# Performance work log

Hardware: AMD Instinct MI355X
Metric: run time of the kernel (lower is better)

The kernel has to match this reference:

```python
import jax, jax.numpy as jnp
import numpy as np
import math

DIM = 512
HID = 2048
BS, SLEN = 4, 4096


def _bayes_linear(x, mu, log_sigma, eps):
    # torchbnn BayesLinear: W = mu + exp(log_sigma) * eps; y = x @ W^T
    W = mu + jnp.exp(log_sigma) * eps
    return jnp.einsum('...i,oi->...o', x, W)


def setup_inputs() -> dict:
    key = jax.random.key(0)
    ks = jax.random.split(key, 20)
    d = {}
    d['x'] = jax.random.normal(ks[0], (BS, SLEN, DIM), dtype=jnp.float32)
    # causal additive mask, broadcast over batch
    causal = jnp.triu(jnp.full((SLEN, SLEN), -1e9, dtype=jnp.float32), k=1)
    d['mask'] = causal[None, :, :]
    shapes = {'wk': (DIM, DIM), 'wv': (DIM, DIM), 'wo': (DIM, DIM), 'w1': (HID, DIM), 'w2': (DIM, HID)}
    i = 1
    for name, shp in shapes.items():
        fan_in = shp[1]
        d[name + '_mu'] = jax.random.normal(ks[i], shp, dtype=jnp.float32) / np.sqrt(fan_in); i += 1
        d[name + '_ls'] = (-3.0 + 0.1 * jax.random.normal(ks[i], shp, dtype=jnp.float32)); i += 1
        d[name + '_eps'] = jax.random.normal(ks[i], shp, dtype=jnp.float32); i += 1
    return d


def reference(x, mask, wk_mu, wk_ls, wk_eps, wv_mu, wv_ls, wv_eps, wo_mu, wo_ls, wo_eps,
              w1_mu, w1_ls, w1_eps, w2_mu, w2_ls, w2_eps):
    dim = x.shape[-1]
    # attention: W_q is identity
    xq = x
    xk = _bayes_linear(x, wk_mu, wk_ls, wk_eps)
    xv = _bayes_linear(x, wv_mu, wv_ls, wv_eps)
    scores = jnp.einsum('bqd,bkd->bqk', xq, xk) / math.sqrt(dim) + mask
    attn = jax.nn.softmax(scores, axis=-1)
    h = jnp.einsum('bqk,bkd->bqd', attn, xv)
    h_attn = _bayes_linear(h, wo_mu, wo_ls, wo_eps)
    h_res = x + h_attn
    # FFN with ReLU
    ff = _bayes_linear(h_res, w1_mu, w1_ls, w1_eps)
    ff = jax.nn.relu(ff)
    ff = _bayes_linear(ff, w2_mu, w2_ls, w2_eps)
    return h_res + ff
```

## Files before the change

### kernel.cpp

```cpp
#include <hip/hip_runtime.h>
#include <hip/hip_bf16.h>

typedef __hip_bfloat16 bf16;
typedef __attribute__((ext_vector_type(8))) short short8;
typedef __attribute__((ext_vector_type(4))) float f32x4;

#define MFMA16(a,b,c) __builtin_amdgcn_mfma_f32_16x16x32_bf16(a,b,c,0,0,0)

__device__ __forceinline__ void gl_lds16(const void* g, void* l) {
  __builtin_amdgcn_global_load_lds(
      (const __attribute__((address_space(1))) void*)g,
      (__attribute__((address_space(3))) void*)l, 16, 0, 0);
}

__global__ __launch_bounds__(256) void prep_kernel(
    const float* __restrict__ x,
    const float* __restrict__ m0, const float* __restrict__ l0, const float* __restrict__ e0,
    const float* __restrict__ m1, const float* __restrict__ l1, const float* __restrict__ e1,
    const float* __restrict__ m2, const float* __restrict__ l2, const float* __restrict__ e2,
    const float* __restrict__ m3, const float* __restrict__ l3, const float* __restrict__ e3,
    const float* __restrict__ m4, const float* __restrict__ l4, const float* __restrict__ e4,
    bf16* __restrict__ xb, bf16* __restrict__ wts)
{
  long e = ((long)blockIdx.x * 256 + threadIdx.x) * 4;
  if (e < 8388608L) {
    float4 v = *(const float4*)(x + e);
    union { bf16 b[4]; short4 s; } u;
    u.b[0] = __float2bfloat16(v.x); u.b[1] = __float2bfloat16(v.y);
    u.b[2] = __float2bfloat16(v.z); u.b[3] = __float2bfloat16(v.w);
    *(short4*)(xb + e) = u.s;
  } else {
    long we = e - 8388608L;
    const float *mu, *ls, *ep; long off = we;
    if (we < 262144L)        { mu = m0; ls = l0; ep = e0; }
    else if (we < 524288L)   { mu = m1; ls = l1; ep = e1; off = we - 262144L; }
    else if (we < 786432L)   { mu = m2; ls = l2; ep = e2; off = we - 524288L; }
    else if (we < 1835008L)  { mu = m3; ls = l3; ep = e3; off = we - 786432L; }
    else                     { mu = m4; ls = l4; ep = e4; off = we - 1835008L; }
    float4 a = *(const float4*)(mu + off);
    float4 b = *(const float4*)(ls + off);
    float4 c = *(const float4*)(ep + off);
    union { bf16 w[4]; short4 s; } u;
    u.w[0] = __float2bfloat16(a.x + __expf(b.x) * c.x);
    u.w[1] = __float2bfloat16(a.y + __expf(b.y) * c.y);
    u.w[2] = __float2bfloat16(a.z + __expf(b.z) * c.z);
    u.w[3] = __float2bfloat16(a.w + __expf(b.w) * c.w);
    *(short4*)(wts + we) = u.s;
  }
}

template<int MODE>
__global__ __launch_bounds__(256, 2) void gemm_nt(
    const bf16* __restrict__ A, const bf16* __restrict__ B,
    const float* __restrict__ resid, float* __restrict__ outf,
    bf16* __restrict__ outb, int M, int N, int K)
{
  __shared__ bf16 As[128 * 32];
  __shared__ bf16 Bs[128 * 32];
  const int t = threadIdx.x, w = t >> 6, lane = t & 63;
  const int quad = lane >> 4, c16 = lane & 15;
  const int bm = blockIdx.x << 7, bn = blockIdx.y << 7;
  const int wr = (w >> 1) << 6, wc = (w & 1) << 6;

  f32x4 acc[4][4] = {};

  const int srow = t >> 2;
  const int scol = (t & 3) * 8;
  const bf16* Ab = A + (long)bm * K;
  const bf16* Bb = B + (long)bn * K;

  for (int k0 = 0; k0 < K; k0 += 32) {
    gl_lds16(Ab + (long)srow * K + k0 + scol,        (char*)As + (w << 10));
    gl_lds16(Ab + (long)(64 + srow) * K + k0 + scol, (char*)As + 4096 + (w << 10));
    gl_lds16(Bb + (long)srow * K + k0 + scol,        (char*)Bs + (w << 10));
    gl_lds16(Bb + (long)(64 + srow) * K + k0 + scol, (char*)Bs + 4096 + (w << 10));
    __syncthreads();
    short8 a[4], b[4];
    #pragma unroll
    for (int i = 0; i < 4; i++)
      a[i] = *(const short8*)(As + (wr + i * 16 + c16) * 32 + quad * 8);
    #pragma unroll
    for (int j = 0; j < 4; j++)
      b[j] = *(const short8*)(Bs + (wc + j * 16 + c16) * 32 + quad * 8);
    #pragma unroll
    for (int i = 0; i < 4; i++)
      #pragma unroll
      for (int j = 0; j < 4; j++)
        acc[i][j] = MFMA16(a[i], b[j], acc[i][j]);
    __syncthreads();
  }

  #pragma unroll
  for (int i = 0; i < 4; i++) {
    const int row = bm + wr + i * 16 + quad * 4;
    #pragma unroll
    for (int j = 0; j < 4; j++) {
      const int col = bn + wc + j * 16 + c16;
      #pragma unroll
      for (int r = 0; r < 4; r++) {
        float v = acc[i][j][r];
        if (MODE == 4) {
          int n = (row + r) & 31;
          long idx = (long)(row + r) * 512 + ((((col >> 3) ^ (n & 7)) << 3) | (col & 7));
          outb[idx] = __float2bfloat16(v);
        } else if (MODE == 5) {
          int g = row + r;
          int kvl = g & 31;
          long idx = (((long)(g >> 5)) << 14) + (long)col * 32 +
                     (((kvl >> 3) ^ ((col >> 1) & 3)) << 3) + (kvl & 7);
          outb[idx] = __float2bfloat16(v);
        } else {
          long idx = (long)(row + r) * N + col;
          if (MODE == 0) {
            outb[idx] = __float2bfloat16(v);
          } else if (MODE == 1) {
            float vv = v + resid[idx];
            outf[idx] = vv;
            outb[idx] = __float2bfloat16(vv);
          } else if (MODE == 2) {
            outb[idx] = __float2bfloat16(v > 0.f ? v : 0.f);
          } else {
            outf[idx] = v + resid[idx];
          }
        }
      }
    }
  }
}

__global__ __launch_bounds__(256, 2) void attn4_kernel(
    const bf16* __restrict__ xq, const bf16* __restrict__ xkS,
    const bf16* __restrict__ xvS, bf16* __restrict__ Opart,
    float* __restrict__ lsum)
{
  __shared__ bf16 Ks[32 * 512];
  __shared__ bf16 Vs[512 * 32];
  __shared__ bf16 Pb[4 * 512];

  const int t = threadIdx.x, w = t >> 6, lane = t & 63;
  const int quad = lane >> 4, c16 = lane & 15;
  const int n = blockIdx.x;
  const int B = n & 3, par = (n >> 2) & 3, i = n >> 4;
  const long boff = (long)B * (4096L * 512);
  const float scale = 0.04419417382415922f;
  const float FM = 30.0f;

  union { short8 s; short u[8]; } ones;
  #pragma unroll
  for (int k = 0; k < 8; k++) ones.u[k] = (short)0x3F80;

  for (int seg = 0; seg < 2; seg++) {
    const int qt = seg ? (63 - i) : i;
    const int T = 2 * (qt + 1);
    const int qb = qt << 6;

    short8 qf[16];
    {
      const bf16* qrow = xq + boff + (long)(qb + w * 16 + c16) * 512 + quad * 8;
      #pragma unroll
      for (int f = 0; f < 16; f++) qf[f] = *(const short8*)(qrow + f * 32);
    }

    f32x4 o[32];
    #pragma unroll
    for (int jj = 0; jj < 32; jj++) o[jj] = (f32x4){0.f, 0.f, 0.f, 0.f};
    f32x4 lacc = (f32x4){0.f, 0.f, 0.f, 0.f};

    for (int tile = par; tile < T; tile += 4) {
      const int kv0 = tile << 5;
      {
        const long tb = ((long)(B * 128 + tile)) << 14;
        const bf16* ks = xkS + tb + (w << 9) + (lane << 3);
        const bf16* vs = xvS + tb + (w << 9) + (lane << 3);
        char* kd = (char*)Ks + (w << 10);
        char* vd = (char*)Vs + (w << 10);
        #pragma unroll
        for (int r2 = 0; r2 < 8; r2++) {
          gl_lds16(ks + (r2 << 11), kd + (r2 << 12));
          gl_lds16(vs + (r2 << 11), vd + (r2 << 12));
        }
      }
      __syncthreads();

      f32x4 s0 = (f32x4){0.f, 0.f, 0.f, 0.f};
      f32x4 s1 = s0;
      const int n0 = c16, n1 = 16 + c16;
      const int sw0 = (c16 & 7) << 3;
      #pragma unroll
      for (int f = 0; f < 16; f++) {
        int cb = (f * 4 + quad) << 3;
        short8 b0 = *(const short8*)(Ks + n0 * 512 + (cb ^ sw0));
        short8 b1 = *(const short8*)(Ks + n1 * 512 + (cb ^ sw0));
        s0 = MFMA16(qf[f], b0, s0);
        s1 = MFMA16(qf[f], b1, s1);
      }

      bf16* Pw = Pb + (w << 9);
      {
        const int qr0 = qb + w * 16 + quad * 4;
        const bool need_mask = (kv0 + 32 > qb);
        #pragma unroll
        for (int r = 0; r < 4; r++) {
          float p0 = __expf(fmaf(s0[r], scale, -FM));
          float p1 = __expf(fmaf(s1[r], scale, -FM));
          if (need_mask) {
            if (kv0 + n0 > qr0 + r) p0 = 0.f;
            if (kv0 + n1 > qr0 + r) p1 = 0.f;
          }
          int pr = quad * 4 + r;
          int swp = (pr >> 1) & 3;
          Pw[pr * 32 + (((n0 >> 3) ^ swp) << 3) + (n0 & 7)] = __float2bfloat16(p0);
          Pw[pr * 32 + (((n1 >> 3) ^ swp) << 3) + (n1 & 7)] = __float2bfloat16(p1);
        }
      }
      short8 pa = *(const short8*)(Pw + c16 * 32 + ((quad ^ ((c16 >> 1) & 3)) << 3));
      lacc = MFMA16(pa, ones.s, lacc);
      #pragma unroll
      for (int jj = 0; jj < 32; jj++) {
        int d = jj * 16 + c16;
        short8 vb = *(const short8*)(Vs + d * 32 + ((quad ^ ((d >> 1) & 3)) << 3));
        o[jj] = MFMA16(pa, vb, o[jj]);
      }
      __syncthreads();
    }

    const int pidx = (B * 64 + qt) * 4 + par;
    {
      bf16* ob = Opart + ((long)pidx << 15) + (long)(w * 16 + quad * 4) * 512 + c16;
      #pragma unroll
      for (int r = 0; r < 4; r++) {
        #pragma unroll
        for (int jj = 0; jj < 32; jj++)
          ob[(long)r * 512 + jj * 16] = __float2bfloat16(o[jj][r]);
      }
      if (c16 == 0) {
        #pragma unroll
        for (int r = 0; r < 4; r++)
          lsum[pidx * 64 + w * 16 + quad * 4 + r] = lacc[r];
      }
    }
  }
}

__global__ __launch_bounds__(256) void combine_kernel(
    const bf16* __restrict__ Opart, const float* __restrict__ lsum,
    bf16* __restrict__ hb)
{
  const int t = threadIdx.x;
  const int r = blockIdx.x * 4 + (t >> 6);
  const int B = r >> 12, rl = r & 4095, qt = rl >> 6, rr = rl & 63;
  const int p0 = (B * 64 + qt) * 4;
  float lt = lsum[p0 * 64 + rr] + lsum[(p0 + 1) * 64 + rr] +
             lsum[(p0 + 2) * 64 + rr] + lsum[(p0 + 3) * 64 + rr];
  float inv = 1.0f / lt;
  const int d0 = (t & 63) * 8;
  union { short8 s; bf16 b[8]; } u0, u1, u2, u3, uo;
  u0.s = *(const short8*)(Opart + (((long)(p0 + 0) << 6) + rr) * 512 + d0);
  u1.s = *(const short8*)(Opart + (((long)(p0 + 1) << 6) + rr) * 512 + d0);
  u2.s = *(const short8*)(Opart + (((long)(p0 + 2) << 6) + rr) * 512 + d0);
  u3.s = *(const short8*)(Opart + (((long)(p0 + 3) << 6) + rr) * 512 + d0);
  #pragma unroll
  for (int k = 0; k < 8; k++) {
    float s = __bfloat162float(u0.b[k]) + __bfloat162float(u1.b[k]) +
              __bfloat162float(u2.b[k]) + __bfloat162float(u3.b[k]);
    uo.b[k] = __float2bfloat16(s * inv);
  }
  *(short8*)(hb + (long)r * 512 + d0) = uo.s;
}

extern "C" void kernel_launch(void* const* d_in, const int* in_sizes, int n_in,
                              void* d_out, int out_size, void* d_ws, size_t ws_size,
                              hipStream_t stream) {
  (void)in_sizes; (void)n_in; (void)out_size; (void)ws_size;
  const float* x = (const float*)d_in[0];
  const float* wk_mu = (const float*)d_in[2],  *wk_ls = (const float*)d_in[3],  *wk_eps = (const float*)d_in[4];
  const float* wv_mu = (const float*)d_in[5],  *wv_ls = (const float*)d_in[6],  *wv_eps = (const float*)d_in[7];
  const float* wo_mu = (const float*)d_in[8],  *wo_ls = (const float*)d_in[9],  *wo_eps = (const float*)d_in[10];
  const float* w1_mu = (const float*)d_in[11], *w1_ls = (const float*)d_in[12], *w1_eps = (const float*)d_in[13];
  const float* w2_mu = (const float*)d_in[14], *w2_ls = (const float*)d_in[15], *w2_eps = (const float*)d_in[16];

  const long MB = 1048576L;
  char* ws = (char*)d_ws;
  bf16*   xb    = (bf16*)(ws + 0);
  bf16*   xkS   = (bf16*)(ws + 16 * MB);
  bf16*   xvS   = (bf16*)(ws + 32 * MB);
  bf16*   Opart = (bf16*)(ws + 48 * MB);
  float*  lsb   = (float*)(ws + 112 * MB);
  bf16*   wts   = (bf16*)(ws + 113 * MB);
  bf16*   hb    = (bf16*)(ws + 32 * MB);
  float*  hrf   = (float*)(ws + 64 * MB);
  bf16*   hrb   = (bf16*)(ws + 96 * MB);
  bf16*   ffb   = (bf16*)(ws + 0);

  bf16* wkb = wts;
  bf16* wvb = wts + 262144;
  bf16* wob = wts + 524288;
  bf16* w1b = wts + 786432;
  bf16* w2b = wts + 1835008;

  prep_kernel<<<11008, 256, 0, stream>>>(x,
      wk_mu, wk_ls, wk_eps, wv_mu, wv_ls, wv_eps, wo_mu, wo_ls, wo_eps,
      w1_mu, w1_ls, w1_eps, w2_mu, w2_ls, w2_eps, xb, wts);

  gemm_nt<4><<<dim3(128, 4),  256, 0, stream>>>(xb,  wkb, nullptr, nullptr, xkS, 16384, 512, 512);
  gemm_nt<5><<<dim3(128, 4),  256, 0, stream>>>(xb,  wvb, nullptr, nullptr, xvS, 16384, 512, 512);

  attn4_kernel<<<512, 256, 0, stream>>>(xb, xkS, xvS, Opart, lsb);
  combine_kernel<<<4096, 256, 0, stream>>>(Opart, lsb, hb);

  gemm_nt<1><<<dim3(128, 4),  256, 0, stream>>>(hb,  wob, x,   hrf, hrb, 16384, 512, 512);
  gemm_nt<2><<<dim3(128, 16), 256, 0, stream>>>(hrb, w1b, nullptr, nullptr, ffb, 16384, 2048, 512);
  gemm_nt<3><<<dim3(128, 4),  256, 0, stream>>>(ffb, w2b, hrf, (float*)d_out, nullptr, 16384, 512, 2048);
}
```

Baseline: 464.6 us.

## Prefetch next K/V tiles during compute and split PV output across waves by column

The attention kernel now loads the next tile's K into LDS while the current PV product runs, and the next V right after it finishes, so global-to-LDS loads overlap with MFMA work. The PV product is repartitioned: each wave reads the P tiles of all four waves from LDS and owns a 128-column slice of the output for all 64 rows. Each V fragment is then read from LDS once and reused across four row blocks, instead of every wave reading all of V. This adds extra barriers and P reads per tile, and it changes the Opart write pattern.

```diff
diff --git a/kernel.cpp b/kernel.cpp
--- a/kernel.cpp
+++ b/kernel.cpp
@@ -128,7 +128,7 @@
   }
 }
 
-__global__ __launch_bounds__(256, 2) void attn4_kernel(
+__global__ __launch_bounds__(256, 2) void attn5_kernel(
     const bf16* __restrict__ xq, const bf16* __restrict__ xkS,
     const bf16* __restrict__ xvS, bf16* __restrict__ Opart,
     float* __restrict__ lsum)
@@ -149,6 +149,21 @@
   #pragma unroll
   for (int k = 0; k < 8; k++) ones.u[k] = (short)0x3F80;
 
+  auto stageK = [&](int tile) {
+    const long tb = ((long)(B * 128 + tile)) << 14;
+    const bf16* ks = xkS + tb + (w << 9) + (lane << 3);
+    char* kd = (char*)Ks + (w << 10);
+    #pragma unroll
+    for (int r2 = 0; r2 < 8; r2++) gl_lds16(ks + (r2 << 11), kd + (r2 << 12));
+  };
+  auto stageV = [&](int tile) {
+    const long tb = ((long)(B * 128 + tile)) << 14;
+    const bf16* vs = xvS + tb + (w << 9) + (lane << 3);
+    char* vd = (char*)Vs + (w << 10);
+    #pragma unroll
+    for (int r2 = 0; r2 < 8; r2++) gl_lds16(vs + (r2 << 11), vd + (r2 << 12));
+  };
+
   for (int seg = 0; seg < 2; seg++) {
     const int qt = seg ? (63 - i) : i;
     const int T = 2 * (qt + 1);
@@ -161,25 +176,17 @@
       for (int f = 0; f < 16; f++) qf[f] = *(const short8*)(qrow + f * 32);
     }
 
-    f32x4 o[32];
-    #pragma unroll
-    for (int jj = 0; jj < 32; jj++) o[jj] = (f32x4){0.f, 0.f, 0.f, 0.f};
+    f32x4 o[4][8];
+    #pragma unroll
+    for (int rb = 0; rb < 4; rb++)
+      #pragma unroll
+      for (int db = 0; db < 8; db++) o[rb][db] = (f32x4){0.f, 0.f, 0.f, 0.f};
     f32x4 lacc = (f32x4){0.f, 0.f, 0.f, 0.f};
+
+    if (par < T) { stageK(par); stageV(par); }
 
     for (int tile = par; tile < T; tile += 4) {
       const int kv0 = tile << 5;
-      {
-        const long tb = ((long)(B * 128 + tile)) << 14;
-        const bf16* ks = xkS + tb + (w << 9) + (lane << 3);
-        const bf16* vs = xvS + tb + (w << 9) + (lane << 3);
-        char* kd = (char*)Ks + (w << 10);
-        char* vd = (char*)Vs + (w << 10);
-        #pragma unroll
-        for (int r2 = 0; r2 < 8; r2++) {
-          gl_lds16(ks + (r2 << 11), kd + (r2 << 12));
-          gl_lds16(vs + (r2 << 11), vd + (r2 << 12));
-        }
-      }
       __syncthreads();
 
       f32x4 s0 = (f32x4){0.f, 0.f, 0.f, 0.f};
@@ -195,8 +202,8 @@
         s1 = MFMA16(qf[f], b1, s1);
       }
 
-      bf16* Pw = Pb + (w << 9);
       {
+        bf16* Pw = Pb + (w << 9);
         const int qr0 = qb + w * 16 + quad * 4;
         const bool need_mask = (kv0 + 32 > qb);
         #pragma unroll
@@ -213,25 +220,45 @@
           Pw[pr * 32 + (((n1 >> 3) ^ swp) << 3) + (n1 & 7)] = __float2bfloat16(p1);
         }
       }
-      short8 pa = *(const short8*)(Pw + c16 * 32 + ((quad ^ ((c16 >> 1) & 3)) << 3));
-      lacc = MFMA16(pa, ones.s, lacc);
-      #pragma unroll
-      for (int jj = 0; jj < 32; jj++) {
-        int d = jj * 16 + c16;
-        short8 vb = *(const short8*)(Vs + d * 32 + ((quad ^ ((d >> 1) & 3)) << 3));
-        o[jj] = MFMA16(pa, vb, o[jj]);
-      }
       __syncthreads();
+      const bool nxt = (tile + 4) < T;
+      if (nxt) stageK(tile + 4);
+
+      {
+        const int prd = ((quad ^ ((c16 >> 1) & 3)) << 3);
+        short8 pf[4];
+        #pragma unroll
+        for (int rb = 0; rb < 4; rb++)
+          pf[rb] = *(const short8*)(Pb + (rb << 9) + c16 * 32 + prd);
+        short8 pown = *(const short8*)(Pb + (w << 9) + c16 * 32 + prd);
+        lacc = MFMA16(pown, ones.s, lacc);
+        #pragma unroll
+        for (int db = 0; db < 8; db++) {
+          int d = (w << 7) + (db << 4) + c16;
+          short8 vb = *(const short8*)(Vs + d * 32 + ((quad ^ ((d >> 1) & 3)) << 3));
+          #pragma unroll
+          for (int rb = 0; rb < 4; rb++)
+            o[rb][db] = MFMA16(pf[rb], vb, o[rb][db]);
+        }
+      }
+      __syncthreads();
+      if (nxt) stageV(tile + 4);
     }
 
     const int pidx = (B * 64 + qt) * 4 + par;
     {
-      bf16* ob = Opart + ((long)pidx << 15) + (long)(w * 16 + quad * 4) * 512 + c16;
-      #pragma unroll
-      for (int r = 0; r < 4; r++) {
-        #pragma unroll
-        for (int jj = 0; jj < 32; jj++)
-          ob[(long)r * 512 + jj * 16] = __float2bfloat16(o[jj][r]);
+      bf16* ob = Opart + ((long)pidx << 15);
+      #pragma unroll
+      for (int rb = 0; rb < 4; rb++) {
+        #pragma unroll
+        for (int r = 0; r < 4; r++) {
+          const int row = rb * 16 + quad * 4 + r;
+          #pragma unroll
+          for (int db = 0; db < 8; db++) {
+            const int col = (w << 7) + (db << 4) + c16;
+            ob[(long)row * 512 + col] = __float2bfloat16(o[rb][db][r]);
+          }
+        }
       }
       if (c16 == 0) {
         #pragma unroll
@@ -239,6 +266,7 @@
           lsum[pidx * 64 + w * 16 + quad * 4 + r] = lacc[r];
       }
     }
+    __syncthreads();
   }
 }
 
@@ -305,7 +333,7 @@
   gemm_nt<4><<<dim3(128, 4),  256, 0, stream>>>(xb,  wkb, nullptr, nullptr, xkS, 16384, 512, 512);
   gemm_nt<5><<<dim3(128, 4),  256, 0, stream>>>(xb,  wvb, nullptr, nullptr, xvS, 16384, 512, 512);
 
-  attn4_kernel<<<512, 256, 0, stream>>>(xb, xkS, xvS, Opart, lsb);
+  attn5_kernel<<<512, 256, 0, stream>>>(xb, xkS, xvS, Opart, lsb);
   combine_kernel<<<4096, 256, 0, stream>>>(Opart, lsb, hb);
 
   gemm_nt<1><<<dim3(128, 4),  256, 0, stream>>>(hb,  wob, x,   hrf, hrb, 16384, 512, 512);
```

Measured after the change: 538.2 us. 1.16x slower.

## Double GEMM K-tile to 64 with XOR-swizzled LDS layout

Applied to the files above, without the earlier changes.

The NT GEMM now stages a 128x64 K-slice of A and B per iteration instead of 128x32. This halves the number of barrier pairs and loop iterations, and each sync is followed by 32 MFMAs per wave. The 16-byte chunks are XOR-swizzled by row when loaded into LDS so that the fragment reads avoid bank conflicts. LDS use doubles to 32 KB per block, which may limit occupancy with two blocks per CU. The kernel also assumes K is a multiple of 64.

```diff
diff --git a/kernel.cpp b/kernel.cpp
--- a/kernel.cpp
+++ b/kernel.cpp
@@ -55,8 +55,8 @@
     const float* __restrict__ resid, float* __restrict__ outf,
     bf16* __restrict__ outb, int M, int N, int K)
 {
-  __shared__ bf16 As[128 * 32];
-  __shared__ bf16 Bs[128 * 32];
+  __shared__ bf16 As[128 * 64];
+  __shared__ bf16 Bs[128 * 64];
   const int t = threadIdx.x, w = t >> 6, lane = t & 63;
   const int quad = lane >> 4, c16 = lane & 15;
   const int bm = blockIdx.x << 7, bn = blockIdx.y << 7;
@@ -64,29 +64,37 @@
 
   f32x4 acc[4][4] = {};
 
-  const int srow = t >> 2;
-  const int scol = (t & 3) * 8;
+  const int lh = lane >> 3, l8 = lane & 7;
+  const int gcol = (l8 ^ lh) << 3;
   const bf16* Ab = A + (long)bm * K;
   const bf16* Bb = B + (long)bn * K;
 
-  for (int k0 = 0; k0 < K; k0 += 32) {
-    gl_lds16(Ab + (long)srow * K + k0 + scol,        (char*)As + (w << 10));
-    gl_lds16(Ab + (long)(64 + srow) * K + k0 + scol, (char*)As + 4096 + (w << 10));
-    gl_lds16(Bb + (long)srow * K + k0 + scol,        (char*)Bs + (w << 10));
-    gl_lds16(Bb + (long)(64 + srow) * K + k0 + scol, (char*)Bs + 4096 + (w << 10));
+  for (int k0 = 0; k0 < K; k0 += 64) {
+    #pragma unroll
+    for (int r2 = 0; r2 < 4; r2++) {
+      const int R0 = r2 * 32 + w * 8;
+      gl_lds16(Ab + (long)(R0 + lh) * K + k0 + gcol, (char*)As + R0 * 128);
+      gl_lds16(Bb + (long)(R0 + lh) * K + k0 + gcol, (char*)Bs + R0 * 128);
+    }
     __syncthreads();
-    short8 a[4], b[4];
-    #pragma unroll
-    for (int i = 0; i < 4; i++)
-      a[i] = *(const short8*)(As + (wr + i * 16 + c16) * 32 + quad * 8);
-    #pragma unroll
-    for (int j = 0; j < 4; j++)
-      b[j] = *(const short8*)(Bs + (wc + j * 16 + c16) * 32 + quad * 8);
-    #pragma unroll
-    for (int i = 0; i < 4; i++)
-      #pragma unroll
-      for (int j = 0; j < 4; j++)
-        acc[i][j] = MFMA16(a[i], b[j], acc[i][j]);
+    short8 a[2][4], b[2][4];
+    const int sw = c16 & 7;
+    #pragma unroll
+    for (int i = 0; i < 4; i++) {
+      const int ra = (wr + i * 16 + c16) * 64;
+      const int rb = (wc + i * 16 + c16) * 64;
+      a[0][i] = *(const short8*)(As + ra + ((quad ^ sw) << 3));
+      a[1][i] = *(const short8*)(As + ra + (((quad + 4) ^ sw) << 3));
+      b[0][i] = *(const short8*)(Bs + rb + ((quad ^ sw) << 3));
+      b[1][i] = *(const short8*)(Bs + rb + (((quad + 4) ^ sw) << 3));
+    }
+    #pragma unroll
+    for (int kk = 0; kk < 2; kk++)
+      #pragma unroll
+      for (int i = 0; i < 4; i++)
+        #pragma unroll
+        for (int j = 0; j < 4; j++)
+          acc[i][j] = MFMA16(a[kk][i], b[kk][j], acc[i][j]);
     __syncthreads();
   }
 
```

Result: no change. 464.8 us (+0.0%).
